# Optimization experiments

Measured on AMD Instinct MI355X. Metric: run time of the kernel, lower is better.

Reference implementation:

```python
import jax, jax.numpy as jnp
import numpy as np

N = 50000
E = 600000
IN_C = 128
OUT_C = 64
HID = 2 * OUT_C  # 128


def setup_inputs() -> dict:
    key = jax.random.key(0)
    ks = jax.random.split(key, 8)
    x = jax.random.normal(ks[0], (N, IN_C), dtype=jnp.float32)
    edge_index = jax.random.randint(ks[1], (2, E), 0, N, dtype=jnp.int64)
    # Glorot-style init for GCN weights, zero bias (PyG default)
    def glorot(k, fan_in, fan_out):
        s = jnp.sqrt(6.0 / (fan_in + fan_out)).astype(jnp.float32)
        return jax.random.uniform(k, (fan_in, fan_out), jnp.float32, -s, s)
    return {
        "x": x,
        "edge_index": edge_index,
        "W1": glorot(ks[2], IN_C, HID),
        "b1": jnp.zeros((HID,), jnp.float32),
        "W_mu": glorot(ks[3], HID, OUT_C),
        "b_mu": jnp.zeros((OUT_C,), jnp.float32),
        "W_ls": glorot(ks[4], HID, OUT_C),
        "b_ls": jnp.zeros((OUT_C,), jnp.float32),
    }


def _gcn_norm(edge_index, num_nodes):
    # Add self-loops, compute symmetric normalization (cached=True in original
    # means this is computed once and reused by all three convs -- same math).
    loop = jnp.arange(num_nodes, dtype=edge_index.dtype)
    row = jnp.concatenate([edge_index[0], loop])  # source
    col = jnp.concatenate([edge_index[1], loop])  # target
    deg = jax.ops.segment_sum(jnp.ones_like(col, dtype=jnp.float32), col,
                              num_segments=num_nodes)
    dis = jnp.where(deg > 0, jax.lax.rsqrt(deg), 0.0)  # deg^{-1/2}, inf->0
    norm = dis[row] * dis[col]  # [E+N]
    return row, col, norm


def _gcn_conv(x, W, b, row, col, norm, num_nodes):
    h = x @ W                                  # dense transform [N, out]
    msg = h[row] * norm[:, None]               # gather + scale [E+N, out]
    out = jax.ops.segment_sum(msg, col, num_segments=num_nodes)
    return out + b


def reference(x, edge_index, W1, b1, W_mu, b_mu, W_ls, b_ls):
    num_nodes = x.shape[0]
    row, col, norm = _gcn_norm(edge_index, num_nodes)
    # eval mode: F.dropout is identity when not training
    h = jax.nn.relu(_gcn_conv(x, W1, b1, row, col, norm, num_nodes))
    mu = _gcn_conv(h, W_mu, b_mu, row, col, norm, num_nodes)
    logstd = _gcn_conv(h, W_ls, b_ls, row, col, norm, num_nodes)
    return mu, logstd
```

## Files before the change

### kernel.cpp

```cpp
#include <hip/hip_runtime.h>
#include <hip/hip_fp16.h>


#define N_NODES 50000
#define N_EDGES 600000
#define MU_SIZE (N_NODES * 64)
#define SCAN_BLOCKS 200
#define SCAN_CHUNK 250
#define WT_S 136

typedef _Float16 half8 __attribute__((ext_vector_type(8)));
typedef _Float16 half4 __attribute__((ext_vector_type(4)));
typedef float floatx4 __attribute__((ext_vector_type(4)));

union H8 { __half2 h2[4]; float4 f4; };

__global__ __launch_bounds__(256) void count_kernel(const int* __restrict__ col,
                                                    int* __restrict__ counts, int e) {
  int i = blockIdx.x * 256 + threadIdx.x;
  if (i < e) atomicAdd(&counts[col[i]], 1);
}

__global__ __launch_bounds__(256) void blocksum_dis_kernel(const int* __restrict__ counts,
                                                           float* __restrict__ dis,
                                                           int* __restrict__ blocksums) {
  __shared__ int red[4];
  int b = blockIdx.x, t = threadIdx.x;
  int i = b * SCAN_CHUNK + t;
  int c = 0;
  if (t < SCAN_CHUNK) {
    c = counts[i];
    dis[i] = rsqrtf((float)(c + 1));
  }
  int s = c;
#pragma unroll
  for (int off = 32; off > 0; off >>= 1) s += __shfl_down(s, off, 64);
  if ((t & 63) == 0) red[t >> 6] = s;
  __syncthreads();
  if (t == 0) blocksums[b] = red[0] + red[1] + red[2] + red[3];
}

__global__ __launch_bounds__(256) void offsets_kernel(const int* __restrict__ counts,
                                                      const int* __restrict__ blocksums,
                                                      int* __restrict__ offsets) {
  __shared__ int sb[256];
  __shared__ int loc[256];
  int b = blockIdx.x, t = threadIdx.x;
  sb[t] = (t < SCAN_BLOCKS) ? blocksums[t] : 0;
  __syncthreads();
#pragma unroll
  for (int off = 1; off < 256; off <<= 1) {
    int v = (t >= off) ? sb[t - off] : 0;
    __syncthreads();
    sb[t] += v;
    __syncthreads();
  }
  int base = (b == 0) ? 0 : sb[b - 1];
  int i = b * SCAN_CHUNK + t;
  int c = (t < SCAN_CHUNK) ? counts[i] : 0;
  loc[t] = c;
  __syncthreads();
#pragma unroll
  for (int off = 1; off < 256; off <<= 1) {
    int v = (t >= off) ? loc[t - off] : 0;
    __syncthreads();
    loc[t] += v;
    __syncthreads();
  }
  if (t < SCAN_CHUNK) offsets[i] = base + loc[t] - c;
  if (b == SCAN_BLOCKS - 1 && t == SCAN_CHUNK - 1) offsets[N_NODES] = base + loc[t];
}

__global__ __launch_bounds__(256) void fill_kernel(const int* __restrict__ row,
                                                   const int* __restrict__ col,
                                                   const int* __restrict__ offsets,
                                                   int* __restrict__ fillcnt,
                                                   int* __restrict__ srcidx, int e) {
  int i = blockIdx.x * 256 + threadIdx.x;
  if (i < e) {
    int c = col[i];
    int pos = offsets[c] + atomicAdd(&fillcnt[c], 1);
    srcidx[pos] = row[i];
  }
}

__global__ __launch_bounds__(256) void prep_wt_kernel(const float* __restrict__ W1,
                                                      const float* __restrict__ Wmu,
                                                      const float* __restrict__ Wls,
                                                      _Float16* __restrict__ W1T,
                                                      _Float16* __restrict__ W2T) {
  int idx = blockIdx.x * 256 + threadIdx.x;
  int e = idx & 16383;
  int n = e >> 7, k = e & 127;
  if (idx < 16384) {
    W1T[e] = (_Float16)W1[k * 128 + n];
  } else {
    float w = (n < 64) ? Wmu[k * 64 + n] : Wls[k * 64 + (n - 64)];
    W2T[e] = (_Float16)w;
  }
}

template <bool SPLIT>
__global__ __launch_bounds__(256) void gemm_mfma_kernel(const float* __restrict__ X,
                                                        const _Float16* __restrict__ Xh,
                                                        const _Float16* __restrict__ WT,
                                                        const float* __restrict__ dis,
                                                        const float* __restrict__ ba,
                                                        const float* __restrict__ bb,
                                                        _Float16* __restrict__ Yh,
                                                        float* __restrict__ Yf) {
  __shared__ _Float16 WL[128 * WT_S];

  int t = threadIdx.x;
  for (int idx = t; idx < 128 * 16; idx += 256) {
    int n = idx >> 4, kk = (idx & 15) * 8;
    *(half8*)&WL[n * WT_S + kk] = *(const half8*)&WT[n * 128 + kk];
  }
  __syncthreads();

  int wid = t >> 6, lane = t & 63;
  int q = lane >> 4, m = lane & 15;
  const int ngroups = (N_NODES + 63) / 64;

  for (int g64 = blockIdx.x; g64 < ngroups; g64 += gridDim.x) {
    int node = g64 * 64 + wid * 16 + m;
    size_t nr = (size_t)min(node, N_NODES - 1);
    bool valid = node < N_NODES;

    half8 xfrag[4];
    if (!SPLIT) {
#pragma unroll
      for (int c = 0; c < 4; ++c) {
        const float* ap = &X[nr * 128 + 32 * c + 8 * q];
        float4 a0 = *(const float4*)ap;
        float4 a1 = *(const float4*)(ap + 4);
        half8 af = {(_Float16)a0.x, (_Float16)a0.y, (_Float16)a0.z, (_Float16)a0.w,
                    (_Float16)a1.x, (_Float16)a1.y, (_Float16)a1.z, (_Float16)a1.w};
        xfrag[c] = af;
      }
    } else {
#pragma unroll
      for (int c = 0; c < 4; ++c) {
        xfrag[c] = *(const half8*)&Xh[nr * 128 + 32 * c + 8 * q];
      }
    }
    float dnode = SPLIT ? 0.f : dis[nr];

#pragma unroll
    for (int f = 0; f < 8; ++f) {
      floatx4 acc = {0.f, 0.f, 0.f, 0.f};
#pragma unroll
      for (int c = 0; c < 4; ++c) {
        half8 wfrag = *(const half8*)&WL[(16 * f + m) * WT_S + 32 * c + 8 * q];
        acc = __builtin_amdgcn_mfma_f32_16x16x32_f16(wfrag, xfrag[c], acc, 0, 0, 0);
      }
      int fbase = 16 * f + 4 * q;
      if (!SPLIT) {
        if (valid) {
          half4 o = {(_Float16)(acc[0] * dnode), (_Float16)(acc[1] * dnode),
                     (_Float16)(acc[2] * dnode), (_Float16)(acc[3] * dnode)};
          *(half4*)&Yh[(size_t)node * 128 + fbase] = o;
        }
      } else {
        float4 bias = (f < 4) ? *(const float4*)&ba[fbase]
                              : *(const float4*)&bb[fbase - 64];
        float4 o = make_float4(acc[0] + bias.x, acc[1] + bias.y, acc[2] + bias.z,
                               acc[3] + bias.w);
        if (valid) {
          if (f < 4)
            *(float4*)&Yf[(size_t)node * 64 + fbase] = o;
          else
            *(float4*)&Yf[MU_SIZE + (size_t)node * 64 + (fbase - 64)] = o;
        }
      }
    }
  }
}

template <bool BIAS_RELU>
__global__ __launch_bounds__(256) void aggregate_kernel(const __half* __restrict__ Hs,
                                                        const int* __restrict__ offsets,
                                                        const int* __restrict__ srcidx,
                                                        const float* __restrict__ dis,
                                                        const float* __restrict__ bias,
                                                        __half* __restrict__ outH, int n) {
  int wid = threadIdx.x >> 6, lane = threadIdx.x & 63;
  int q = lane >> 4, ql = lane & 15;
  int i = blockIdx.x * 16 + wid * 4 + q;
  if (i >= n) return;
  float di = dis[i];
  float4 selfv = ((const float4*)(Hs + (size_t)i * 128))[ql];
  float acc[8] = {0.f, 0.f, 0.f, 0.f, 0.f, 0.f, 0.f, 0.f};
  int k = offsets[i], end = offsets[i + 1];
  for (; k + 3 < end; k += 4) {
    int r0 = srcidx[k];
    int r1 = srcidx[k + 1];
    int r2 = srcidx[k + 2];
    int r3 = srcidx[k + 3];
    float4 v0 = ((const float4*)(Hs + (size_t)r0 * 128))[ql];
    float4 v1 = ((const float4*)(Hs + (size_t)r1 * 128))[ql];
    float4 v2 = ((const float4*)(Hs + (size_t)r2 * 128))[ql];
    float4 v3 = ((const float4*)(Hs + (size_t)r3 * 128))[ql];
    const __half2* a0 = (const __half2*)&v0;
    const __half2* a1 = (const __half2*)&v1;
    const __half2* a2 = (const __half2*)&v2;
    const __half2* a3 = (const __half2*)&v3;
#pragma unroll
    for (int j = 0; j < 4; ++j) {
      float2 f0 = __half22float2(a0[j]);
      float2 f1 = __half22float2(a1[j]);
      float2 f2 = __half22float2(a2[j]);
      float2 f3 = __half22float2(a3[j]);
      acc[2 * j] += (f0.x + f1.x) + (f2.x + f3.x);
      acc[2 * j + 1] += (f0.y + f1.y) + (f2.y + f3.y);
    }
  }
  for (; k < end; ++k) {
    int r0 = srcidx[k];
    float4 v0 = ((const float4*)(Hs + (size_t)r0 * 128))[ql];
    const __half2* a0 = (const __half2*)&v0;
#pragma unroll
    for (int j = 0; j < 4; ++j) {
      float2 f0 = __half22float2(a0[j]);
      acc[2 * j] += f0.x;
      acc[2 * j + 1] += f0.y;
    }
  }
  const __half2* sh = (const __half2*)&selfv;
  float s[8];
#pragma unroll
  for (int j = 0; j < 4; ++j) {
    float2 f = __half22float2(sh[j]);
    s[2 * j] = di * (acc[2 * j] + f.x);
    s[2 * j + 1] = di * (acc[2 * j + 1] + f.y);
  }
  H8 u;
  if (BIAS_RELU) {
    float4 b0 = ((const float4*)bias)[2 * ql];
    float4 b1 = ((const float4*)bias)[2 * ql + 1];
    u.h2[0] = __float22half2_rn(
        make_float2(di * fmaxf(s[0] + b0.x, 0.f), di * fmaxf(s[1] + b0.y, 0.f)));
    u.h2[1] = __float22half2_rn(
        make_float2(di * fmaxf(s[2] + b0.z, 0.f), di * fmaxf(s[3] + b0.w, 0.f)));
    u.h2[2] = __float22half2_rn(
        make_float2(di * fmaxf(s[4] + b1.x, 0.f), di * fmaxf(s[5] + b1.y, 0.f)));
    u.h2[3] = __float22half2_rn(
        make_float2(di * fmaxf(s[6] + b1.z, 0.f), di * fmaxf(s[7] + b1.w, 0.f)));
  } else {
    u.h2[0] = __float22half2_rn(make_float2(s[0], s[1]));
    u.h2[1] = __float22half2_rn(make_float2(s[2], s[3]));
    u.h2[2] = __float22half2_rn(make_float2(s[4], s[5]));
    u.h2[3] = __float22half2_rn(make_float2(s[6], s[7]));
  }
  ((float4*)(outH + (size_t)i * 128))[ql] = u.f4;
}

extern "C" void kernel_launch(void* const* d_in, const int* in_sizes, int n_in,
                              void* d_out, int out_size, void* d_ws, size_t ws_size,
                              hipStream_t stream) {
  const float* x = (const float*)d_in[0];
  const int* ei = (const int*)d_in[1];
  const float* W1 = (const float*)d_in[2];
  const float* b1 = (const float*)d_in[3];
  const float* Wmu = (const float*)d_in[4];
  const float* bmu = (const float*)d_in[5];
  const float* Wls = (const float*)d_in[6];
  const float* bls = (const float*)d_in[7];
  float* out = (float*)d_out;

  const int* row = ei;
  const int* col = ei + N_EDGES;

  __half* bufAh = (__half*)d_ws;
  __half* bufBh = bufAh + 6400000;
  __half* bufCh = bufBh + 6400000;
  float* dis = (float*)(bufCh + 6400000);
  int* counts = (int*)(dis + N_NODES);
  int* fillcnt = counts + N_NODES;
  int* offsets = fillcnt + N_NODES;
  int* srcidx = offsets + N_NODES + 1;
  int* blocksums = srcidx + N_EDGES;
  _Float16* W1T = (_Float16*)(blocksums + 256);
  _Float16* W2T = W1T + 16384;

  hipMemsetAsync(counts, 0, 2 * N_NODES * sizeof(int), stream);

  prep_wt_kernel<<<128, 256, 0, stream>>>(W1, Wmu, Wls, W1T, W2T);

  int eb = (N_EDGES + 255) / 256;
  count_kernel<<<eb, 256, 0, stream>>>(col, counts, N_EDGES);
  blocksum_dis_kernel<<<SCAN_BLOCKS, 256, 0, stream>>>(counts, dis, blocksums);
  offsets_kernel<<<SCAN_BLOCKS, 256, 0, stream>>>(counts, blocksums, offsets);
  fill_kernel<<<eb, 256, 0, stream>>>(row, col, offsets, fillcnt, srcidx, N_EDGES);

  gemm_mfma_kernel<false><<<512, 256, 0, stream>>>(x, nullptr, W1T, dis, nullptr, nullptr,
                                                   (_Float16*)bufAh, nullptr);
  int ab = (N_NODES + 15) / 16;
  aggregate_kernel<true><<<ab, 256, 0, stream>>>(bufAh, offsets, srcidx, dis, b1,
                                                 bufBh, N_NODES);
  aggregate_kernel<false><<<ab, 256, 0, stream>>>(bufBh, offsets, srcidx, dis,
                                                  nullptr, bufCh, N_NODES);
  gemm_mfma_kernel<true><<<512, 256, 0, stream>>>(nullptr, (const _Float16*)bufCh, W2T,
                                                  nullptr, bmu, bls, nullptr, out);
}
```

Baseline: 222.1 us.

## Pad CSR rows to multiples of eight with zero-row sentinel and batch gathers

Each node's neighbour list is padded to a multiple of 8 using a sentinel index that points at an extra zero row appended to each feature buffer. The aggregate kernel then issues 8 independent gathers per step with no tail loop, and each 16-lane group handles two nodes at once to raise memory-level parallelism. The memset is folded into the prep kernel. This adds padding work (up to about 7 wasted gathers per node, hitting a cached zero row) and extra registers per thread.

```diff
diff --git a/kernel.cpp b/kernel.cpp
--- a/kernel.cpp
+++ b/kernel.cpp
@@ -8,6 +8,7 @@
 #define SCAN_BLOCKS 200
 #define SCAN_CHUNK 250
 #define WT_S 136
+#define PAD_CAP 960000
 
 typedef _Float16 half8 __attribute__((ext_vector_type(8)));
 typedef _Float16 half4 __attribute__((ext_vector_type(4)));
@@ -27,12 +28,13 @@
   __shared__ int red[4];
   int b = blockIdx.x, t = threadIdx.x;
   int i = b * SCAN_CHUNK + t;
-  int c = 0;
+  int dp = 0;
   if (t < SCAN_CHUNK) {
-    c = counts[i];
+    int c = counts[i];
     dis[i] = rsqrtf((float)(c + 1));
-  }
-  int s = c;
+    dp = (c + 7) & ~7;
+  }
+  int s = dp;
 #pragma unroll
   for (int off = 32; off > 0; off >>= 1) s += __shfl_down(s, off, 64);
   if ((t & 63) == 0) red[t >> 6] = s;
@@ -42,7 +44,8 @@
 
 __global__ __launch_bounds__(256) void offsets_kernel(const int* __restrict__ counts,
                                                       const int* __restrict__ blocksums,
-                                                      int* __restrict__ offsets) {
+                                                      int* __restrict__ offsets,
+                                                      int* __restrict__ srcidx) {
   __shared__ int sb[256];
   __shared__ int loc[256];
   int b = blockIdx.x, t = threadIdx.x;
@@ -57,8 +60,12 @@
   }
   int base = (b == 0) ? 0 : sb[b - 1];
   int i = b * SCAN_CHUNK + t;
-  int c = (t < SCAN_CHUNK) ? counts[i] : 0;
-  loc[t] = c;
+  int c = 0, dp = 0;
+  if (t < SCAN_CHUNK) {
+    c = counts[i];
+    dp = (c + 7) & ~7;
+  }
+  loc[t] = dp;
   __syncthreads();
 #pragma unroll
   for (int off = 1; off < 256; off <<= 1) {
@@ -67,7 +74,11 @@
     loc[t] += v;
     __syncthreads();
   }
-  if (t < SCAN_CHUNK) offsets[i] = base + loc[t] - c;
+  if (t < SCAN_CHUNK) {
+    int off0 = base + loc[t] - dp;
+    offsets[i] = off0;
+    for (int z = c; z < dp; ++z) srcidx[off0 + z] = N_NODES;
+  }
   if (b == SCAN_BLOCKS - 1 && t == SCAN_CHUNK - 1) offsets[N_NODES] = base + loc[t];
 }
 
@@ -84,12 +95,20 @@
   }
 }
 
-__global__ __launch_bounds__(256) void prep_wt_kernel(const float* __restrict__ W1,
-                                                      const float* __restrict__ Wmu,
-                                                      const float* __restrict__ Wls,
-                                                      _Float16* __restrict__ W1T,
-                                                      _Float16* __restrict__ W2T) {
+__global__ __launch_bounds__(256) void prep_kernel(const float* __restrict__ W1,
+                                                   const float* __restrict__ Wmu,
+                                                   const float* __restrict__ Wls,
+                                                   _Float16* __restrict__ W1T,
+                                                   _Float16* __restrict__ W2T,
+                                                   int* __restrict__ zero2n,
+                                                   __half* __restrict__ zrowA,
+                                                   __half* __restrict__ zrowB) {
   int idx = blockIdx.x * 256 + threadIdx.x;
+  for (int z = idx; z < 2 * N_NODES; z += 32768) zero2n[z] = 0;
+  if (idx < 128) {
+    zrowA[idx] = __float2half(0.f);
+    zrowB[idx] = __float2half(0.f);
+  }
   int e = idx & 16383;
   int n = e >> 7, k = e & 127;
   if (idx < 16384) {
@@ -186,73 +205,100 @@
                                                         __half* __restrict__ outH, int n) {
   int wid = threadIdx.x >> 6, lane = threadIdx.x & 63;
   int q = lane >> 4, ql = lane & 15;
-  int i = blockIdx.x * 16 + wid * 4 + q;
-  if (i >= n) return;
-  float di = dis[i];
-  float4 selfv = ((const float4*)(Hs + (size_t)i * 128))[ql];
-  float acc[8] = {0.f, 0.f, 0.f, 0.f, 0.f, 0.f, 0.f, 0.f};
-  int k = offsets[i], end = offsets[i + 1];
-  for (; k + 3 < end; k += 4) {
-    int r0 = srcidx[k];
-    int r1 = srcidx[k + 1];
-    int r2 = srcidx[k + 2];
-    int r3 = srcidx[k + 3];
-    float4 v0 = ((const float4*)(Hs + (size_t)r0 * 128))[ql];
-    float4 v1 = ((const float4*)(Hs + (size_t)r1 * 128))[ql];
-    float4 v2 = ((const float4*)(Hs + (size_t)r2 * 128))[ql];
-    float4 v3 = ((const float4*)(Hs + (size_t)r3 * 128))[ql];
-    const __half2* a0 = (const __half2*)&v0;
-    const __half2* a1 = (const __half2*)&v1;
-    const __half2* a2 = (const __half2*)&v2;
-    const __half2* a3 = (const __half2*)&v3;
-#pragma unroll
-    for (int j = 0; j < 4; ++j) {
-      float2 f0 = __half22float2(a0[j]);
-      float2 f1 = __half22float2(a1[j]);
-      float2 f2 = __half22float2(a2[j]);
-      float2 f3 = __half22float2(a3[j]);
-      acc[2 * j] += (f0.x + f1.x) + (f2.x + f3.x);
-      acc[2 * j + 1] += (f0.y + f1.y) + (f2.y + f3.y);
-    }
-  }
-  for (; k < end; ++k) {
-    int r0 = srcidx[k];
-    float4 v0 = ((const float4*)(Hs + (size_t)r0 * 128))[ql];
-    const __half2* a0 = (const __half2*)&v0;
-#pragma unroll
-    for (int j = 0; j < 4; ++j) {
-      float2 f0 = __half22float2(a0[j]);
-      acc[2 * j] += f0.x;
-      acc[2 * j + 1] += f0.y;
-    }
-  }
-  const __half2* sh = (const __half2*)&selfv;
-  float s[8];
-#pragma unroll
-  for (int j = 0; j < 4; ++j) {
-    float2 f = __half22float2(sh[j]);
-    s[2 * j] = di * (acc[2 * j] + f.x);
-    s[2 * j + 1] = di * (acc[2 * j + 1] + f.y);
-  }
-  H8 u;
-  if (BIAS_RELU) {
-    float4 b0 = ((const float4*)bias)[2 * ql];
-    float4 b1 = ((const float4*)bias)[2 * ql + 1];
-    u.h2[0] = __float22half2_rn(
-        make_float2(di * fmaxf(s[0] + b0.x, 0.f), di * fmaxf(s[1] + b0.y, 0.f)));
-    u.h2[1] = __float22half2_rn(
-        make_float2(di * fmaxf(s[2] + b0.z, 0.f), di * fmaxf(s[3] + b0.w, 0.f)));
-    u.h2[2] = __float22half2_rn(
-        make_float2(di * fmaxf(s[4] + b1.x, 0.f), di * fmaxf(s[5] + b1.y, 0.f)));
-    u.h2[3] = __float22half2_rn(
-        make_float2(di * fmaxf(s[6] + b1.z, 0.f), di * fmaxf(s[7] + b1.w, 0.f)));
-  } else {
-    u.h2[0] = __float22half2_rn(make_float2(s[0], s[1]));
-    u.h2[1] = __float22half2_rn(make_float2(s[2], s[3]));
-    u.h2[2] = __float22half2_rn(make_float2(s[4], s[5]));
-    u.h2[3] = __float22half2_rn(make_float2(s[6], s[7]));
-  }
-  ((float4*)(outH + (size_t)i * 128))[ql] = u.f4;
+  int base = blockIdx.x * 32 + wid * 8;
+  int i0 = base + q, i1 = base + q + 4;
+  int k0 = 0, e0 = 0, k1 = 0, e1 = 0;
+  if (i0 < n) {
+    k0 = offsets[i0];
+    e0 = offsets[i0 + 1];
+  }
+  if (i1 < n) {
+    k1 = offsets[i1];
+    e1 = offsets[i1 + 1];
+  }
+  float accA[8] = {0.f, 0.f, 0.f, 0.f, 0.f, 0.f, 0.f, 0.f};
+  float accB[8] = {0.f, 0.f, 0.f, 0.f, 0.f, 0.f, 0.f, 0.f};
+  while ((k0 < e0) || (k1 < e1)) {
+    bool g0 = k0 < e0, g1 = k1 < e1;
+    float4 vA[8], vB[8];
+    if (g0) {
+#pragma unroll
+      for (int u = 0; u < 8; ++u) {
+        int r = srcidx[k0 + u];
+        vA[u] = ((const float4*)(Hs + (size_t)r * 128))[ql];
+      }
+    }
+    if (g1) {
+#pragma unroll
+      for (int u = 0; u < 8; ++u) {
+        int r = srcidx[k1 + u];
+        vB[u] = ((const float4*)(Hs + (size_t)r * 128))[ql];
+      }
+    }
+    if (g0) {
+#pragma unroll
+      for (int u = 0; u < 8; ++u) {
+        const __half2* a = (const __half2*)&vA[u];
+#pragma unroll
+        for (int j = 0; j < 4; ++j) {
+          float2 f = __half22float2(a[j]);
+          accA[2 * j] += f.x;
+          accA[2 * j + 1] += f.y;
+        }
+      }
+      k0 += 8;
+    }
+    if (g1) {
+#pragma unroll
+      for (int u = 0; u < 8; ++u) {
+        const __half2* a = (const __half2*)&vB[u];
+#pragma unroll
+        for (int j = 0; j < 4; ++j) {
+          float2 f = __half22float2(a[j]);
+          accB[2 * j] += f.x;
+          accB[2 * j + 1] += f.y;
+        }
+      }
+      k1 += 8;
+    }
+  }
+
+#pragma unroll
+  for (int which = 0; which < 2; ++which) {
+    int i = which ? i1 : i0;
+    const float* acc = which ? accB : accA;
+    if (i < n) {
+      float di = dis[i];
+      float4 selfv = ((const float4*)(Hs + (size_t)i * 128))[ql];
+      const __half2* sh = (const __half2*)&selfv;
+      float s[8];
+#pragma unroll
+      for (int j = 0; j < 4; ++j) {
+        float2 f = __half22float2(sh[j]);
+        s[2 * j] = di * (acc[2 * j] + f.x);
+        s[2 * j + 1] = di * (acc[2 * j + 1] + f.y);
+      }
+      H8 u;
+      if (BIAS_RELU) {
+        float4 b0 = ((const float4*)bias)[2 * ql];
+        float4 b1 = ((const float4*)bias)[2 * ql + 1];
+        u.h2[0] = __float22half2_rn(
+            make_float2(di * fmaxf(s[0] + b0.x, 0.f), di * fmaxf(s[1] + b0.y, 0.f)));
+        u.h2[1] = __float22half2_rn(
+            make_float2(di * fmaxf(s[2] + b0.z, 0.f), di * fmaxf(s[3] + b0.w, 0.f)));
+        u.h2[2] = __float22half2_rn(
+            make_float2(di * fmaxf(s[4] + b1.x, 0.f), di * fmaxf(s[5] + b1.y, 0.f)));
+        u.h2[3] = __float22half2_rn(
+            make_float2(di * fmaxf(s[6] + b1.z, 0.f), di * fmaxf(s[7] + b1.w, 0.f)));
+      } else {
+        u.h2[0] = __float22half2_rn(make_float2(s[0], s[1]));
+        u.h2[1] = __float22half2_rn(make_float2(s[2], s[3]));
+        u.h2[2] = __float22half2_rn(make_float2(s[4], s[5]));
+        u.h2[3] = __float22half2_rn(make_float2(s[6], s[7]));
+      }
+      ((float4*)(outH + (size_t)i * 128))[ql] = u.f4;
+    }
+  }
 }
 
 extern "C" void kernel_launch(void* const* d_in, const int* in_sizes, int n_in,
@@ -272,30 +318,30 @@
   const int* col = ei + N_EDGES;
 
   __half* bufAh = (__half*)d_ws;
-  __half* bufBh = bufAh + 6400000;
-  __half* bufCh = bufBh + 6400000;
+  __half* bufBh = bufAh + 6400128;
+  __half* bufCh = bufBh + 6400128;
   float* dis = (float*)(bufCh + 6400000);
   int* counts = (int*)(dis + N_NODES);
   int* fillcnt = counts + N_NODES;
   int* offsets = fillcnt + N_NODES;
   int* srcidx = offsets + N_NODES + 1;
-  int* blocksums = srcidx + N_EDGES;
+  int* blocksums = srcidx + PAD_CAP;
   _Float16* W1T = (_Float16*)(blocksums + 256);
   _Float16* W2T = W1T + 16384;
 
-  hipMemsetAsync(counts, 0, 2 * N_NODES * sizeof(int), stream);
-
-  prep_wt_kernel<<<128, 256, 0, stream>>>(W1, Wmu, Wls, W1T, W2T);
+  prep_kernel<<<128, 256, 0, stream>>>(W1, Wmu, Wls, W1T, W2T, counts,
+                                       bufAh + (size_t)N_NODES * 128,
+                                       bufBh + (size_t)N_NODES * 128);
 
   int eb = (N_EDGES + 255) / 256;
   count_kernel<<<eb, 256, 0, stream>>>(col, counts, N_EDGES);
   blocksum_dis_kernel<<<SCAN_BLOCKS, 256, 0, stream>>>(counts, dis, blocksums);
-  offsets_kernel<<<SCAN_BLOCKS, 256, 0, stream>>>(counts, blocksums, offsets);
+  offsets_kernel<<<SCAN_BLOCKS, 256, 0, stream>>>(counts, blocksums, offsets, srcidx);
   fill_kernel<<<eb, 256, 0, stream>>>(row, col, offsets, fillcnt, srcidx, N_EDGES);
 
   gemm_mfma_kernel<false><<<512, 256, 0, stream>>>(x, nullptr, W1T, dis, nullptr, nullptr,
                                                    (_Float16*)bufAh, nullptr);
-  int ab = (N_NODES + 15) / 16;
+  int ab = (N_NODES + 31) / 32;
   aggregate_kernel<true><<<ab, 256, 0, stream>>>(bufAh, offsets, srcidx, dis, b1,
                                                  bufBh, N_NODES);
   aggregate_kernel<false><<<ab, 256, 0, stream>>>(bufBh, offsets, srcidx, dis,
```

After: 228.9 us. 3.1% more time.
